# Performance work log

Measured on AMD Instinct MI355X. Metric: run time of the kernel, lower is better.

## Reference

```python
import jax, jax.numpy as jnp
import numpy as np

# Model constants (buffers in the torch module)
TAU_S, TAU_M, TAU_A = 5.0, 10.0, 20.0
R_GAIN, KAPPA, W_BG, NU_BG = 1.5, 0.2, 0.1, 1.0
N = 2048   # num_neurons
T = 2048   # number of time points
DT = 0.005


def setup_inputs() -> dict:
    key = jax.random.key(0)
    k1, k2, k3 = jax.random.split(key, 3)
    t = jnp.arange(T, dtype=jnp.float32) * DT            # [T] time grid
    state = jax.random.normal(k1, (4, N), dtype=jnp.float32) * 0.1   # [4,N] = (I,H,A,R)
    stim = jax.random.normal(k2, (N,), dtype=jnp.float32) * 0.01     # [N]
    W = jax.random.normal(k3, (N, N), dtype=jnp.float32) * 0.1       # [N,N] recurrent weights
    return {"t": t, "state": state, "stim": stim, "W": W}


def _ode_func(state, stim, W):
    # state: [4, N]
    I, H, A, R = state
    dI = -I / TAU_S + W @ jax.lax.stop_gradient(R) + W_BG * NU_BG + stim
    dH = (-H + R_GAIN * dI) / TAU_M
    dA = (-A + KAPPA * R) / TAU_A
    dR = jnp.tanh(H - A)
    return jnp.stack([dI, dH, dA, dR])


def reference(t, state, stim, W):
    """Fixed-step RK4 integration over the time grid t (odeint equivalent).
    Returns trajectory [T, 4, N] including the initial state."""
    f = lambda y: _ode_func(y, stim, W)
    dts = t[1:] - t[:-1]  # [T-1]

    def step(y, dt):
        k1 = f(y)
        k2 = f(y + 0.5 * dt * k1)
        k3 = f(y + 0.5 * dt * k2)
        k4 = f(y + dt * k3)
        y = y + (dt / 6.0) * (k1 + 2.0 * k2 + 2.0 * k3 + k4)
        return y, y

    _, traj = jax.lax.scan(step, state, dts)
    return jnp.concatenate([state[None], traj], axis=0)
```

## Files before the change

kernel.cpp:

```cpp
#include <hip/hip_runtime.h>
#include <cstdint>
#include <cstddef>


#define NWG    64
#define TPB    512
#define NN     2048
#define TT     2048
#define ROWS   32
#define NP     ((TT - 1) * 2)
#define FPAD   64

__global__ __launch_bounds__(TPB, 2)
void node_rk4_kernel(const float* __restrict__ tgrid,
                     const float* __restrict__ state0,
                     const float* __restrict__ stim,
                     const float* __restrict__ W,
                     float* __restrict__ out,
                     float* __restrict__ Rbuf,
                     unsigned* __restrict__ flags)
{
    const int g    = blockIdx.x;
    const int tid  = threadIdx.x;
    const int wave = tid >> 6;
    const int lane = tid & 63;
    const int n0   = g * ROWS;
    const int myrow = n0 + 4 * wave;

    extern __shared__ float lds[];
    float* tg = lds;

    for (int i = tid; i < TT; i += TPB) tg[i] = tgrid[i];

    float4 w[4][8];
    {
        const float4* Wg = reinterpret_cast<const float4*>(W)
                         + (size_t)myrow * (NN / 4);
#pragma unroll
        for (int r = 0; r < 4; ++r)
#pragma unroll
            for (int k = 0; k < 8; ++k)
                w[r][k] = Wg[(size_t)r * (NN / 4) + lane + 64 * k];
    }
    __syncthreads();

    float yI = 0.f, yH = 0.f, yA = 0.f, yR = 0.f, st = 0.f;
    float k1I = 0.f, k1H = 0.f, k1A = 0.f, k1R = 0.f;
    float k2I = 0.f, k2H = 0.f, k2A = 0.f, k2R = 0.f;
    float bI = 0.f, bH = 0.f, bA = 0.f, bR = 0.f;

    if (lane < 4) {
        const int i = myrow + lane;
        yI = state0[0 * NN + i];
        yH = state0[1 * NN + i];
        yA = state0[2 * NN + i];
        yR = state0[3 * NN + i];
        st = stim[i];
        const float dt0 = tg[1] - tg[0];
        Rbuf[0 * NN + i] = yR;
        Rbuf[1 * NN + i] = yR + (0.5f * dt0) * tanhf(yH - yA);
    }
    asm volatile("s_waitcnt vmcnt(0)" ::: "memory");
    __syncthreads();
    if (tid == 0)
        __hip_atomic_store(&flags[(size_t)g * FPAD], 1u,
                           __ATOMIC_RELEASE, __HIP_MEMORY_SCOPE_AGENT);
    if (lane < 4) {
        const int i = myrow + lane;
        out[0 * NN + i] = yI;
        out[1 * NN + i] = yH;
        out[2 * NN + i] = yA;
        out[3 * NN + i] = yR;
    }

    for (int p = 0; p < NP; ++p) {
        const int n = p >> 1;

        {
            const unsigned tgt = (unsigned)p + 1u;
            if (tid < NWG) {
                while (__hip_atomic_load(&flags[(size_t)tid * FPAD],
                                         __ATOMIC_RELAXED,
                                         __HIP_MEMORY_SCOPE_AGENT) < tgt) { }
            }
            __syncthreads();
            __builtin_amdgcn_fence(__ATOMIC_ACQUIRE, "agent");
        }

        const float4* R04 = reinterpret_cast<const float4*>(Rbuf + ((p & 1) * 2 + 0) * NN);
        const float4* R14 = reinterpret_cast<const float4*>(Rbuf + ((p & 1) * 2 + 1) * NN);

        float a0 = 0.f, a1 = 0.f, a2 = 0.f, a3 = 0.f;
        float b0 = 0.f, b1 = 0.f, b2 = 0.f, b3 = 0.f;
#pragma unroll
        for (int k = 0; k < 8; ++k) {
            const int c = lane + 64 * k;
            const float4 ra = R04[c];
            const float4 rb = R14[c];
            a0 += w[0][k].x * ra.x + w[0][k].y * ra.y + w[0][k].z * ra.z + w[0][k].w * ra.w;
            a1 += w[1][k].x * ra.x + w[1][k].y * ra.y + w[1][k].z * ra.z + w[1][k].w * ra.w;
            a2 += w[2][k].x * ra.x + w[2][k].y * ra.y + w[2][k].z * ra.z + w[2][k].w * ra.w;
            a3 += w[3][k].x * ra.x + w[3][k].y * ra.y + w[3][k].z * ra.z + w[3][k].w * ra.w;
            b0 += w[0][k].x * rb.x + w[0][k].y * rb.y + w[0][k].z * rb.z + w[0][k].w * rb.w;
            b1 += w[1][k].x * rb.x + w[1][k].y * rb.y + w[1][k].z * rb.z + w[1][k].w * rb.w;
            b2 += w[2][k].x * rb.x + w[2][k].y * rb.y + w[2][k].z * rb.z + w[2][k].w * rb.w;
            b3 += w[3][k].x * rb.x + w[3][k].y * rb.y + w[3][k].z * rb.z + w[3][k].w * rb.w;
        }
#pragma unroll
        for (int off = 32; off > 0; off >>= 1) {
            a0 += __shfl_xor(a0, off, 64);
            a1 += __shfl_xor(a1, off, 64);
            a2 += __shfl_xor(a2, off, 64);
            a3 += __shfl_xor(a3, off, 64);
            b0 += __shfl_xor(b0, off, 64);
            b1 += __shfl_xor(b1, off, 64);
            b2 += __shfl_xor(b2, off, 64);
            b3 += __shfl_xor(b3, off, 64);
        }

        bool wrote_out = false;
        float oI = 0.f, oH = 0.f, oA = 0.f, oR = 0.f;
        if (lane < 4) {
            const int   r  = lane;
            const float u1 = (r == 0) ? a0 : (r == 1) ? a1 : (r == 2) ? a2 : a3;
            const float u2 = (r == 0) ? b0 : (r == 1) ? b1 : (r == 2) ? b2 : b3;
            const float dt = tg[n + 1] - tg[n];
            const int   i  = myrow + r;
            float* pub = Rbuf + (((p + 1) & 1) * 2) * NN;

            if ((p & 1) == 0) {
                k1I = -yI / 5.0f + u1 + 0.1f + st;
                k1H = (-yH + 1.5f * k1I) / 10.0f;
                k1A = (-yA + 0.2f * yR) / 20.0f;
                k1R = tanhf(yH - yA);
                const float h = 0.5f * dt;
                const float aI_ = yI + h * k1I, aH_ = yH + h * k1H;
                const float aA_ = yA + h * k1A, aR_ = yR + h * k1R;
                k2I = -aI_ / 5.0f + u2 + 0.1f + st;
                k2H = (-aH_ + 1.5f * k2I) / 10.0f;
                k2A = (-aA_ + 0.2f * aR_) / 20.0f;
                k2R = tanhf(aH_ - aA_);
                bI = yI + h * k2I;  bH = yH + h * k2H;
                bA = yA + h * k2A;  bR = yR + h * k2R;
                const float k3R = tanhf(bH - bA);
                pub[i]      = bR;
                pub[NN + i] = yR + dt * k3R;
            } else {
                const float k3I = -bI / 5.0f + u1 + 0.1f + st;
                const float k3H = (-bH + 1.5f * k3I) / 10.0f;
                const float k3A = (-bA + 0.2f * bR) / 20.0f;
                const float k3R = tanhf(bH - bA);
                const float cI = yI + dt * k3I, cH = yH + dt * k3H;
                const float cA = yA + dt * k3A, cR = yR + dt * k3R;
                const float k4I = -cI / 5.0f + u2 + 0.1f + st;
                const float k4H = (-cH + 1.5f * k4I) / 10.0f;
                const float k4A = (-cA + 0.2f * cR) / 20.0f;
                const float k4R = tanhf(cH - cA);
                const float h6 = dt / 6.0f;
                yI = yI + h6 * ((k1I + 2.0f * k2I) + 2.0f * k3I + k4I);
                yH = yH + h6 * ((k1H + 2.0f * k2H) + 2.0f * k3H + k4H);
                yA = yA + h6 * ((k1A + 2.0f * k2A) + 2.0f * k3A + k4A);
                yR = yR + h6 * ((k1R + 2.0f * k2R) + 2.0f * k3R + k4R);
                const float dtn = (n + 2 < TT) ? (tg[n + 2] - tg[n + 1]) : 0.0f;
                pub[i]      = yR;
                pub[NN + i] = yR + (0.5f * dtn) * tanhf(yH - yA);
                oI = yI; oH = yH; oA = yA; oR = yR;
                wrote_out = true;
            }
        }
        asm volatile("s_waitcnt vmcnt(0)" ::: "memory");
        __syncthreads();
        if (tid == 0)
            __hip_atomic_store(&flags[(size_t)g * FPAD], (unsigned)p + 2u,
                               __ATOMIC_RELEASE, __HIP_MEMORY_SCOPE_AGENT);
        if (wrote_out) {
            const int i = myrow + lane;
            float* o = out + (size_t)(n + 1) * 4 * NN;
            o[0 * NN + i] = oI;
            o[1 * NN + i] = oH;
            o[2 * NN + i] = oA;
            o[3 * NN + i] = oR;
        }
    }
}

extern "C" void kernel_launch(void* const* d_in, const int* in_sizes, int n_in,
                              void* d_out, int out_size, void* d_ws, size_t ws_size,
                              hipStream_t stream)
{
    const float* tgrid  = (const float*)d_in[0];
    const float* state0 = (const float*)d_in[1];
    const float* stim   = (const float*)d_in[2];
    const float* W      = (const float*)d_in[3];
    float*       out    = (float*)d_out;

    float*    Rbuf  = (float*)d_ws;
    unsigned* flags = (unsigned*)((char*)d_ws + 4 * NN * sizeof(float));

    hipMemsetAsync(flags, 0, NWG * FPAD * sizeof(unsigned), stream);

    const size_t dyn_lds = 84 * 1024;
    (void)hipFuncSetAttribute((const void*)node_rk4_kernel,
                              hipFuncAttributeMaxDynamicSharedMemorySize,
                              (int)dyn_lds);

    node_rk4_kernel<<<dim3(NWG), dim3(TPB), dyn_lds, stream>>>(
        tgrid, state0, stim, W, out, Rbuf, flags);
}
```

Before: 34.66 ms.

## Replace per-block flag barriers with sequence-tagged R values polled per wave

Drops the per-workgroup flag spin-wait, __syncthreads and release/acquire fences around each RK4 half-step. Each R value is now published as a 64-bit word with the step sequence number in its high half, and each wave polls only the tagged words it consumes until the tags match. The launch becomes 128 blocks of 256 threads, so each wave works and synchronises on its own. This removes a global barrier round-trip per phase but adds wider 8-byte loads, polling traffic on every operand, and a changed memory layout for R.

```diff
diff --git a/kernel.cpp b/kernel.cpp
--- a/kernel.cpp
+++ b/kernel.cpp
@@ -3,39 +3,56 @@
 #include <cstddef>
 
 
-#define NWG    64
-#define TPB    512
-#define NN     2048
-#define TT     2048
-#define ROWS   32
-#define NP     ((TT - 1) * 2)
-#define FPAD   64
-
-__global__ __launch_bounds__(TPB, 2)
+#define NWG   128
+#define TPB   256
+#define WPG   (TPB / 64)
+#define NWAVE (NWG * WPG)
+#define NN    2048
+#define TT    2048
+#define NP    ((TT - 1) * 2)
+
+typedef float f4 __attribute__((ext_vector_type(4)));
+typedef unsigned long long u64;
+
+__device__ __forceinline__ float dot4(const f4 a, const f4 b) {
+    return a.x * b.x + a.y * b.y + a.z * b.z + a.w * b.w;
+}
+
+__device__ __forceinline__ u64 pack_tag(float v, unsigned seq) {
+    return (u64)__float_as_uint(v) | ((u64)seq << 32);
+}
+
+__device__ __forceinline__ u64 tag_load(u64* p) {
+    return __hip_atomic_load(p, __ATOMIC_RELAXED, __HIP_MEMORY_SCOPE_AGENT);
+}
+
+__device__ __forceinline__ void tag_store(u64* p, u64 v) {
+    __hip_atomic_store(p, v, __ATOMIC_RELAXED, __HIP_MEMORY_SCOPE_AGENT);
+}
+
+__global__ __launch_bounds__(TPB, 1)
 void node_rk4_kernel(const float* __restrict__ tgrid,
                      const float* __restrict__ state0,
                      const float* __restrict__ stim,
                      const float* __restrict__ W,
                      float* __restrict__ out,
-                     float* __restrict__ Rbuf,
-                     unsigned* __restrict__ flags)
+                     u64* __restrict__ Rtag)
 {
     const int g    = blockIdx.x;
     const int tid  = threadIdx.x;
     const int wave = tid >> 6;
     const int lane = tid & 63;
-    const int n0   = g * ROWS;
-    const int myrow = n0 + 4 * wave;
+    const int gw   = g * WPG + wave;
+    const int myrow = 4 * gw;
 
     extern __shared__ float lds[];
     float* tg = lds;
 
     for (int i = tid; i < TT; i += TPB) tg[i] = tgrid[i];
 
-    float4 w[4][8];
+    f4 w[4][8];
     {
-        const float4* Wg = reinterpret_cast<const float4*>(W)
-                         + (size_t)myrow * (NN / 4);
+        const f4* Wg = reinterpret_cast<const f4*>(W) + (size_t)myrow * (NN / 4);
 #pragma unroll
         for (int r = 0; r < 4; ++r)
 #pragma unroll
@@ -57,16 +74,9 @@
         yR = state0[3 * NN + i];
         st = stim[i];
         const float dt0 = tg[1] - tg[0];
-        Rbuf[0 * NN + i] = yR;
-        Rbuf[1 * NN + i] = yR + (0.5f * dt0) * tanhf(yH - yA);
-    }
-    asm volatile("s_waitcnt vmcnt(0)" ::: "memory");
-    __syncthreads();
-    if (tid == 0)
-        __hip_atomic_store(&flags[(size_t)g * FPAD], 1u,
-                           __ATOMIC_RELEASE, __HIP_MEMORY_SCOPE_AGENT);
-    if (lane < 4) {
-        const int i = myrow + lane;
+        const float Ra  = yR + (0.5f * dt0) * tanhf(yH - yA);
+        tag_store(Rtag + (size_t)(0 * 4 + lane) * NWAVE + gw, pack_tag(yR, 1u));
+        tag_store(Rtag + (size_t)(4 + lane) * NWAVE + gw,     pack_tag(Ra, 1u));
         out[0 * NN + i] = yI;
         out[1 * NN + i] = yH;
         out[2 * NN + i] = yA;
@@ -75,37 +85,55 @@
 
     for (int p = 0; p < NP; ++p) {
         const int n = p >> 1;
-
-        {
-            const unsigned tgt = (unsigned)p + 1u;
-            if (tid < NWG) {
-                while (__hip_atomic_load(&flags[(size_t)tid * FPAD],
-                                         __ATOMIC_RELAXED,
-                                         __HIP_MEMORY_SCOPE_AGENT) < tgt) { }
-            }
-            __syncthreads();
-            __builtin_amdgcn_fence(__ATOMIC_ACQUIRE, "agent");
-        }
-
-        const float4* R04 = reinterpret_cast<const float4*>(Rbuf + ((p & 1) * 2 + 0) * NN);
-        const float4* R14 = reinterpret_cast<const float4*>(Rbuf + ((p & 1) * 2 + 1) * NN);
+        const unsigned tgt = (unsigned)p + 1u;
+        u64* T0 = Rtag + (size_t)((p & 1) * 8 + 0) * NWAVE;
+        u64* T1 = Rtag + (size_t)((p & 1) * 8 + 4) * NWAVE;
 
         float a0 = 0.f, a1 = 0.f, a2 = 0.f, a3 = 0.f;
         float b0 = 0.f, b1 = 0.f, b2 = 0.f, b3 = 0.f;
+
 #pragma unroll
         for (int k = 0; k < 8; ++k) {
-            const int c = lane + 64 * k;
-            const float4 ra = R04[c];
-            const float4 rb = R14[c];
-            a0 += w[0][k].x * ra.x + w[0][k].y * ra.y + w[0][k].z * ra.z + w[0][k].w * ra.w;
-            a1 += w[1][k].x * ra.x + w[1][k].y * ra.y + w[1][k].z * ra.z + w[1][k].w * ra.w;
-            a2 += w[2][k].x * ra.x + w[2][k].y * ra.y + w[2][k].z * ra.z + w[2][k].w * ra.w;
-            a3 += w[3][k].x * ra.x + w[3][k].y * ra.y + w[3][k].z * ra.z + w[3][k].w * ra.w;
-            b0 += w[0][k].x * rb.x + w[0][k].y * rb.y + w[0][k].z * rb.z + w[0][k].w * rb.w;
-            b1 += w[1][k].x * rb.x + w[1][k].y * rb.y + w[1][k].z * rb.z + w[1][k].w * rb.w;
-            b2 += w[2][k].x * rb.x + w[2][k].y * rb.y + w[2][k].z * rb.z + w[2][k].w * rb.w;
-            b3 += w[3][k].x * rb.x + w[3][k].y * rb.y + w[3][k].z * rb.z + w[3][k].w * rb.w;
-        }
+            const int widx = 64 * k + lane;
+            u64 t0, t1, t2, t3, s0, s1, s2, s3;
+            for (;;) {
+                t0 = tag_load(T0 + 0 * NWAVE + widx);
+                t1 = tag_load(T0 + 1 * NWAVE + widx);
+                t2 = tag_load(T0 + 2 * NWAVE + widx);
+                t3 = tag_load(T0 + 3 * NWAVE + widx);
+                s0 = tag_load(T1 + 0 * NWAVE + widx);
+                s1 = tag_load(T1 + 1 * NWAVE + widx);
+                s2 = tag_load(T1 + 2 * NWAVE + widx);
+                s3 = tag_load(T1 + 3 * NWAVE + widx);
+                const bool ok = ((unsigned)(t0 >> 32) == tgt) &
+                                ((unsigned)(t1 >> 32) == tgt) &
+                                ((unsigned)(t2 >> 32) == tgt) &
+                                ((unsigned)(t3 >> 32) == tgt) &
+                                ((unsigned)(s0 >> 32) == tgt) &
+                                ((unsigned)(s1 >> 32) == tgt) &
+                                ((unsigned)(s2 >> 32) == tgt) &
+                                ((unsigned)(s3 >> 32) == tgt);
+                if (ok) break;
+                __builtin_amdgcn_s_sleep(1);
+            }
+            const f4 ra = { __uint_as_float((unsigned)t0),
+                            __uint_as_float((unsigned)t1),
+                            __uint_as_float((unsigned)t2),
+                            __uint_as_float((unsigned)t3) };
+            const f4 rb = { __uint_as_float((unsigned)s0),
+                            __uint_as_float((unsigned)s1),
+                            __uint_as_float((unsigned)s2),
+                            __uint_as_float((unsigned)s3) };
+            a0 += dot4(w[0][k], ra);
+            a1 += dot4(w[1][k], ra);
+            a2 += dot4(w[2][k], ra);
+            a3 += dot4(w[3][k], ra);
+            b0 += dot4(w[0][k], rb);
+            b1 += dot4(w[1][k], rb);
+            b2 += dot4(w[2][k], rb);
+            b3 += dot4(w[3][k], rb);
+        }
+
 #pragma unroll
         for (int off = 32; off > 0; off >>= 1) {
             a0 += __shfl_xor(a0, off, 64);
@@ -125,8 +153,10 @@
             const float u1 = (r == 0) ? a0 : (r == 1) ? a1 : (r == 2) ? a2 : a3;
             const float u2 = (r == 0) ? b0 : (r == 1) ? b1 : (r == 2) ? b2 : b3;
             const float dt = tg[n + 1] - tg[n];
-            const int   i  = myrow + r;
-            float* pub = Rbuf + (((p + 1) & 1) * 2) * NN;
+            const unsigned seq = (unsigned)p + 2u;
+            u64* P0 = Rtag + (size_t)(((p + 1) & 1) * 8 + r) * NWAVE + gw;
+            u64* P1 = P0 + 4 * NWAVE;
+            float v0, v1;
 
             if ((p & 1) == 0) {
                 k1I = -yI / 5.0f + u1 + 0.1f + st;
@@ -143,8 +173,8 @@
                 bI = yI + h * k2I;  bH = yH + h * k2H;
                 bA = yA + h * k2A;  bR = yR + h * k2R;
                 const float k3R = tanhf(bH - bA);
-                pub[i]      = bR;
-                pub[NN + i] = yR + dt * k3R;
+                v0 = bR;
+                v1 = yR + dt * k3R;
             } else {
                 const float k3I = -bI / 5.0f + u1 + 0.1f + st;
                 const float k3H = (-bH + 1.5f * k3I) / 10.0f;
@@ -162,17 +192,14 @@
                 yA = yA + h6 * ((k1A + 2.0f * k2A) + 2.0f * k3A + k4A);
                 yR = yR + h6 * ((k1R + 2.0f * k2R) + 2.0f * k3R + k4R);
                 const float dtn = (n + 2 < TT) ? (tg[n + 2] - tg[n + 1]) : 0.0f;
-                pub[i]      = yR;
-                pub[NN + i] = yR + (0.5f * dtn) * tanhf(yH - yA);
+                v0 = yR;
+                v1 = yR + (0.5f * dtn) * tanhf(yH - yA);
                 oI = yI; oH = yH; oA = yA; oR = yR;
                 wrote_out = true;
             }
-        }
-        asm volatile("s_waitcnt vmcnt(0)" ::: "memory");
-        __syncthreads();
-        if (tid == 0)
-            __hip_atomic_store(&flags[(size_t)g * FPAD], (unsigned)p + 2u,
-                               __ATOMIC_RELEASE, __HIP_MEMORY_SCOPE_AGENT);
+            tag_store(P0, pack_tag(v0, seq));
+            tag_store(P1, pack_tag(v1, seq));
+        }
         if (wrote_out) {
             const int i = myrow + lane;
             float* o = out + (size_t)(n + 1) * 4 * NN;
@@ -193,11 +220,9 @@
     const float* stim   = (const float*)d_in[2];
     const float* W      = (const float*)d_in[3];
     float*       out    = (float*)d_out;
-
-    float*    Rbuf  = (float*)d_ws;
-    unsigned* flags = (unsigned*)((char*)d_ws + 4 * NN * sizeof(float));
-
-    hipMemsetAsync(flags, 0, NWG * FPAD * sizeof(unsigned), stream);
+    u64*         Rtag   = (u64*)d_ws;
+
+    hipMemsetAsync(Rtag, 0, 2 * 2 * 4 * NWAVE * sizeof(u64), stream);
 
     const size_t dyn_lds = 84 * 1024;
     (void)hipFuncSetAttribute((const void*)node_rk4_kernel,
@@ -205,5 +230,5 @@
                               (int)dyn_lds);
 
     node_rk4_kernel<<<dim3(NWG), dim3(TPB), dyn_lds, stream>>>(
-        tgrid, state0, stim, W, out, Rbuf, flags);
-}
+        tgrid, state0, stim, W, out, Rtag);
+}
```

Measured after the change: 43.27 ms. 24.8% more time.
